# Kernel optimization log

Hardware: AMD Instinct MI355X
Metric: run time of the kernel (lower is better)

## Reference

```python
import jax, jax.numpy as jnp
import numpy as np

NSITES = 100000
NYEARS = 20
NVIS = 2
HDIM = 64


def setup_inputs() -> dict:
    key = jax.random.key(0)
    ks = jax.random.split(key, 10)
    def w(k, shape, fan_in):
        return (jax.random.normal(k, shape, jnp.float32) / np.sqrt(fan_in)).astype(jnp.float32)
    return {
        "sxy0": jax.random.normal(ks[0], (1, NSITES, 1), jnp.float32),
        "sxy": jax.random.normal(ks[1], (NSITES, NYEARS - 1, 1), jnp.float32),
        "oxy": jax.random.normal(ks[2], (NSITES, NYEARS, NVIS), jnp.float32),
        # to_h0: Linear(1 -> 64)
        "W_h0": w(ks[3], (HDIM, 1), 1), "b_h0": jnp.zeros((HDIM,), jnp.float32),
        # to_h1: Linear(64 -> 64)
        "W_h1": w(ks[4], (HDIM, HDIM), HDIM), "b_h1": jnp.zeros((HDIM,), jnp.float32),
        # to_hrnn: RNN(input=1, hidden=64, relu)
        "W_ih": w(ks[5], (HDIM, 1), 1), "b_ih": jnp.zeros((HDIM,), jnp.float32),
        "W_hh": w(ks[6], (HDIM, HDIM), HDIM), "b_hh": jnp.zeros((HDIM,), jnp.float32),
        # to_psi0 / to_psi: Linear(64 -> 1)
        "W_psi0": w(ks[7], (1, HDIM), HDIM), "b_psi0": jnp.zeros((1,), jnp.float32),
        "W_psi": w(ks[8], (1, HDIM), HDIM), "b_psi": jnp.zeros((1,), jnp.float32),
        # to_p: Linear(65 -> 1)
        "W_p": w(ks[9], (1, HDIM + 1), HDIM + 1), "b_p": jnp.zeros((1,), jnp.float32),
    }


def reference(sxy0, sxy, oxy, W_h0, b_h0, W_h1, b_h1, W_ih, b_ih, W_hh, b_hh,
              W_psi0, b_psi0, W_psi, b_psi, W_p, b_p):
    # site embeddings -> initial hidden state
    hs = jax.nn.elu(sxy0 @ W_h0.T + b_h0)            # [1, N, H]
    h0 = jax.nn.elu(hs @ W_h1.T + b_h1)              # [1, N, H]

    # single-layer relu RNN, batch_first: sxy [N, T, 1], h0 [1, N, H]
    xs = jnp.swapaxes(sxy, 0, 1)                     # [T, N, 1]
    def step(h, x):
        h_new = jax.nn.relu(x @ W_ih.T + b_ih + h @ W_hh.T + b_hh)
        return h_new, h_new
    _, h_seq = jax.lax.scan(step, h0[0], xs)         # [T, N, H]
    h_out = jnp.swapaxes(h_seq, 0, 1)                # [N, T, H]

    psi0_out = jax.nn.sigmoid(h0 @ W_psi0.T + b_psi0)   # [1, N, 1]
    psi_out = jax.nn.sigmoid(h_out @ W_psi.T + b_psi)   # [N, T, 1]

    # detection prob p[i, t, j] = sigmoid(to_p(cat(H[i, t], oxy[i, t, j])))
    # where H[:, 0] = h0 and H[:, t] = h_out[:, t-1] for t >= 1
    H = jnp.concatenate([h0[0][:, None, :], h_out], axis=1)  # [N, Y, H]
    logits = H @ W_p[:, :HDIM].T + oxy * W_p[0, HDIM] + b_p  # [N, Y, NVIS]
    p = jax.nn.sigmoid(logits)
    return psi0_out, psi_out, p
```

## Files before the change

kernel.cpp:

```cpp
#include <hip/hip_runtime.h>
#include <math.h>

#define NSITES 100000
#define NYEARS 20
#define HDIM 64
#define WSTR 72
#define SPB 128

typedef __bf16 bf16x8 __attribute__((ext_vector_type(8)));
typedef float f32x4 __attribute__((ext_vector_type(4)));

__device__ __forceinline__ float sigmoidf_(float x) { return 1.0f / (1.0f + __expf(-x)); }
__device__ __forceinline__ float eluf_(float x) { return x > 0.0f ? x : __expf(x) - 1.0f; }

__device__ __forceinline__ unsigned pack2_(float a, float b) {
    union { __bf16 h; unsigned short u; } x, y;
    x.h = (__bf16)a; y.h = (__bf16)b;
    return ((unsigned)y.u << 16) | (unsigned)x.u;
}

__device__ __forceinline__ bf16x8 cvt8_(const float* p) {
    float4 a = ((const float4*)p)[0];
    float4 b = ((const float4*)p)[1];
    bf16x8 r;
    r[0] = (__bf16)a.x; r[1] = (__bf16)a.y; r[2] = (__bf16)a.z; r[3] = (__bf16)a.w;
    r[4] = (__bf16)b.x; r[5] = (__bf16)b.y; r[6] = (__bf16)b.z; r[7] = (__bf16)b.w;
    return r;
}

__device__ __forceinline__ bf16x8 ldsfrag_(const unsigned short* b, int row, int off) {
    union { bf16x8 v; uint4 u; } r;
    r.u = *(const uint4*)&b[row * WSTR + off];
    return r.v;
}

__device__ __forceinline__ bf16x8 pack_bf_(f32x4 lo, f32x4 hi) {
    bf16x8 r;
    r[0] = (__bf16)lo[0]; r[1] = (__bf16)lo[1]; r[2] = (__bf16)lo[2]; r[3] = (__bf16)lo[3];
    r[4] = (__bf16)hi[0]; r[5] = (__bf16)hi[1]; r[6] = (__bf16)hi[2]; r[7] = (__bf16)hi[3];
    return r;
}

__global__ __launch_bounds__(512, 2)
void rnet_kernel(const float* __restrict__ sxy0,
                 const float* __restrict__ sxy,
                 const float* __restrict__ oxy,
                 const float* __restrict__ W_h0, const float* __restrict__ b_h0,
                 const float* __restrict__ W_h1, const float* __restrict__ b_h1,
                 const float* __restrict__ W_ih, const float* __restrict__ b_ih,
                 const float* __restrict__ W_hh, const float* __restrict__ b_hh,
                 const float* __restrict__ W_psi0, const float* __restrict__ b_psi0,
                 const float* __restrict__ W_psi, const float* __restrict__ b_psi,
                 const float* __restrict__ W_p, const float* __restrict__ b_p,
                 float* __restrict__ out)
{
    const int tid  = threadIdx.x;
    const int lane = tid & 63;
    const int wv   = tid >> 6;
    const int s = lane & 15;
    const int q = lane >> 4;
    const int sq = s >> 2, sr = s & 3;
    const int base = blockIdx.x * SPB;
    const int sl   = wv * 16 + s;
    const int site = base + sl;
    const int site_ld = site < NSITES ? site : NSITES - 1;

    __shared__ __align__(16) unsigned char region[SPB * 20 * 2 * 4];
    __shared__ __align__(16) float xs_sh[SPB * 19];
    unsigned short* const whh_l = (unsigned short*)region;
    unsigned short* const wh1_l = (unsigned short*)region + 64 * WSTR;
    float* const pL   = (float*)region;
    float* const psiL = (float*)region + SPB * 20;

    float* __restrict__ out_psi0 = out;
    float* __restrict__ out_psi  = out + NSITES;
    float* __restrict__ out_p    = out + 20 * NSITES;

    {
        const float4* whg = (const float4*)W_hh;
        const float4* w1g = (const float4*)W_h1;
#pragma unroll
        for (int j = 0; j < 2; ++j) {
            int e4 = j * 512 + tid;
            int row = e4 >> 4, c4 = e4 & 15;
            float4 a = whg[e4];
            uint2 pa; pa.x = pack2_(a.x, a.y); pa.y = pack2_(a.z, a.w);
            *(uint2*)&whh_l[row * WSTR + c4 * 4] = pa;
            float4 b = w1g[e4];
            uint2 pb; pb.x = pack2_(b.x, b.y); pb.y = pack2_(b.z, b.w);
            *(uint2*)&wh1_l[row * WSTR + c4 * 4] = pb;
        }
#pragma unroll
        for (int r = 0; r < 5; ++r) {
            int i = r * 512 + tid;
            if (i < SPB * 19) {
                int srow = i / 19, c = i - srow * 19;
                int gsite = base + srow; if (gsite >= NSITES) gsite = NSITES - 1;
                xs_sh[i] = sxy[(size_t)gsite * 19 + c];
            }
        }
    }
    __syncthreads();

    bf16x8 bf[2];
    {
        const float s0v = sxy0[site_ld];
        bf16x8 bf0[2];
#pragma unroll
        for (int kt = 0; kt < 2; ++kt) {
            const float* wp = W_h0 + kt * 32 + q * 8;
            const float* bp = b_h0 + kt * 32 + q * 8;
            float4 w0 = ((const float4*)wp)[0], w1 = ((const float4*)wp)[1];
            float4 c0 = ((const float4*)bp)[0], c1 = ((const float4*)bp)[1];
            float v[8];
            v[0] = eluf_(fmaf(s0v, w0.x, c0.x)); v[1] = eluf_(fmaf(s0v, w0.y, c0.y));
            v[2] = eluf_(fmaf(s0v, w0.z, c0.z)); v[3] = eluf_(fmaf(s0v, w0.w, c0.w));
            v[4] = eluf_(fmaf(s0v, w1.x, c1.x)); v[5] = eluf_(fmaf(s0v, w1.y, c1.y));
            v[6] = eluf_(fmaf(s0v, w1.z, c1.z)); v[7] = eluf_(fmaf(s0v, w1.w, c1.w));
#pragma unroll
            for (int j = 0; j < 8; ++j) bf0[kt][j] = (__bf16)v[j];
        }

        f32x4 acc[4];
#pragma unroll
        for (int mt = 0; mt < 4; ++mt) {
            const int dr = 32 * (mt >> 1) + 8 * q + 4 * (mt & 1);
            float4 b1 = *(const float4*)(b_h1 + dr);
            acc[mt][0] = b1.x; acc[mt][1] = b1.y; acc[mt][2] = b1.z; acc[mt][3] = b1.w;
        }
#pragma unroll
        for (int kt = 0; kt < 2; ++kt)
#pragma unroll
            for (int mt = 0; mt < 4; ++mt) {
                const int ar = 32 * (mt >> 1) + 8 * sq + 4 * (mt & 1) + sr;
                bf16x8 a = ldsfrag_(wh1_l, ar, kt * 32 + q * 8);
                acc[mt] = __builtin_amdgcn_mfma_f32_16x16x32_bf16(a, bf0[kt], acc[mt], 0, 0, 0);
            }
        f32x4 e[4];
#pragma unroll
        for (int mt = 0; mt < 4; ++mt)
#pragma unroll
            for (int r = 0; r < 4; ++r) e[mt][r] = eluf_(acc[mt][r]);
        bf[0] = pack_bf_(e[0], e[1]);
        bf[1] = pack_bf_(e[2], e[3]);
    }

    bf16x8 a_hh[4][2];
#pragma unroll
    for (int mt = 0; mt < 4; ++mt) {
        const int ar = 32 * (mt >> 1) + 8 * sq + 4 * (mt & 1) + sr;
#pragma unroll
        for (int kt = 0; kt < 2; ++kt)
            a_hh[mt][kt] = ldsfrag_(whh_l, ar, kt * 32 + q * 8);
    }

    __syncthreads();

    bf16x8 a_head[2];
    {
        const float* hrow = (s == 1) ? W_p : ((s == 2) ? W_psi0 : W_psi);
#pragma unroll
        for (int kt = 0; kt < 2; ++kt) a_head[kt] = cvt8_(hrow + kt * 32 + q * 8);
    }
    f32x4 biasD[4], wihD[4];
#pragma unroll
    for (int mt = 0; mt < 4; ++mt) {
        const int dr = 32 * (mt >> 1) + 8 * q + 4 * (mt & 1);
        float4 bi = *(const float4*)(b_ih + dr);
        float4 bh = *(const float4*)(b_hh + dr);
        float4 wi = *(const float4*)(W_ih + dr);
        biasD[mt][0] = bi.x + bh.x; biasD[mt][1] = bi.y + bh.y;
        biasD[mt][2] = bi.z + bh.z; biasD[mt][3] = bi.w + bh.w;
        wihD[mt][0] = wi.x; wihD[mt][1] = wi.y; wihD[mt][2] = wi.z; wihD[mt][3] = wi.w;
    }
    f32x4 headC;
    headC[0] = (q == 0) ? b_psi[0]  : 0.0f;
    headC[1] = (q == 0) ? b_p[0]    : 0.0f;
    headC[2] = (q == 0) ? b_psi0[0] : 0.0f;
    headC[3] = 0.0f;

    float x = xs_sh[sl * 19];
#pragma unroll 1
    for (int t = 1; t < NYEARS; ++t) {
        float x_next = (t < NYEARS - 1) ? xs_sh[sl * 19 + t] : 0.0f;

        f32x4 acc[4], accH;
#pragma unroll
        for (int mt = 0; mt < 4; ++mt)
            acc[mt] = __builtin_amdgcn_mfma_f32_16x16x32_bf16(a_hh[mt][0], bf[0], biasD[mt], 0, 0, 0);
        accH = __builtin_amdgcn_mfma_f32_16x16x32_bf16(a_head[0], bf[0], headC, 0, 0, 0);
#pragma unroll
        for (int mt = 0; mt < 4; ++mt)
            acc[mt] = __builtin_amdgcn_mfma_f32_16x16x32_bf16(a_hh[mt][1], bf[1], acc[mt], 0, 0, 0);
        accH = __builtin_amdgcn_mfma_f32_16x16x32_bf16(a_head[1], bf[1], accH, 0, 0, 0);

        f32x4 hn[4];
#pragma unroll
        for (int mt = 0; mt < 4; ++mt)
#pragma unroll
            for (int r = 0; r < 4; ++r)
                hn[mt][r] = fmaxf(fmaf(x, wihD[mt][r], acc[mt][r]), 0.0f);
        bf[0] = pack_bf_(hn[0], hn[1]);
        bf[1] = pack_bf_(hn[2], hn[3]);

        if (q == 0) {
            pL[sl * 20 + (t - 1)]   = accH[1];
            psiL[sl * 20 + (t - 1)] = accH[0];
            if (t == 1) psiL[sl * 20] = accH[2];
        }
        x = x_next;
    }

    {
        f32x4 accH = __builtin_amdgcn_mfma_f32_16x16x32_bf16(a_head[0], bf[0], headC, 0, 0, 0);
        accH = __builtin_amdgcn_mfma_f32_16x16x32_bf16(a_head[1], bf[1], accH, 0, 0, 0);
        if (q == 0) {
            pL[sl * 20 + 19]   = accH[1];
            psiL[sl * 20 + 19] = accH[0];
        }
    }

    __syncthreads();

    const float wpo = W_p[HDIM];
    if (tid < SPB && base + tid < NSITES) out_psi0[base + tid] = sigmoidf_(psiL[tid * 20]);
#pragma unroll
    for (int r = 0; r < 5; ++r) {
        int i = r * 512 + tid;
        if (i < SPB * 19 && (size_t)base * 19 + i < (size_t)NSITES * 19) {
            int s2 = i / 19, c = i - s2 * 19;
            out_psi[(size_t)base * 19 + i] = sigmoidf_(psiL[s2 * 20 + c + 1]);
        }
    }
    const float4* oxy_b = (const float4*)(oxy + (size_t)base * 40);
    float4* outp_b = (float4*)(out_p + (size_t)base * 40);
    const int p4max = (NSITES * 40) / 4;
#pragma unroll
    for (int r = 0; r < 3; ++r) {
        int i4 = r * 512 + tid;
        if (i4 < SPB * 10 && blockIdx.x * (SPB * 10) + i4 < p4max) {
            float4 ox = oxy_b[i4];
            float lg0 = pL[i4 * 2];
            float lg1 = pL[i4 * 2 + 1];
            float4 pv;
            pv.x = sigmoidf_(fmaf(wpo, ox.x, lg0));
            pv.y = sigmoidf_(fmaf(wpo, ox.y, lg0));
            pv.z = sigmoidf_(fmaf(wpo, ox.z, lg1));
            pv.w = sigmoidf_(fmaf(wpo, ox.w, lg1));
            outp_b[i4] = pv;
        }
    }
}

extern "C" void kernel_launch(void* const* d_in, const int* in_sizes, int n_in,
                              void* d_out, int out_size, void* d_ws, size_t ws_size,
                              hipStream_t stream) {
    const float* sxy0   = (const float*)d_in[0];
    const float* sxy    = (const float*)d_in[1];
    const float* oxy    = (const float*)d_in[2];
    const float* W_h0   = (const float*)d_in[3];
    const float* b_h0   = (const float*)d_in[4];
    const float* W_h1   = (const float*)d_in[5];
    const float* b_h1   = (const float*)d_in[6];
    const float* W_ih   = (const float*)d_in[7];
    const float* b_ih   = (const float*)d_in[8];
    const float* W_hh   = (const float*)d_in[9];
    const float* b_hh   = (const float*)d_in[10];
    const float* W_psi0 = (const float*)d_in[11];
    const float* b_psi0 = (const float*)d_in[12];
    const float* W_psi  = (const float*)d_in[13];
    const float* b_psi  = (const float*)d_in[14];
    const float* W_p    = (const float*)d_in[15];
    const float* b_p    = (const float*)d_in[16];

    float* out = (float*)d_out;

    dim3 block(512);
    dim3 grid((NSITES + SPB - 1) / SPB);
    rnet_kernel<<<grid, block, 0, stream>>>(
        sxy0, sxy, oxy, W_h0, b_h0, W_h1, b_h1, W_ih, b_ih, W_hh, b_hh,
        W_psi0, b_psi0, W_psi, b_psi, W_p, b_p, out);
}
```

Measured before the change: 146.7 us.

## Process two independent site groups per wave to interleave RNN recurrences

Halves the block to 256 threads so each wave handles two 16-site groups (A and B), running their recurrent MFMA chains interleaved within the same time step. The intent is to hide the dependent MFMA latency of the serial RNN recurrence by giving the scheduler independent work. Weight fragments in registers are shared between both groups, but register pressure roughly doubles for state and accumulators, and occupancy per block changes.

```diff
diff --git a/kernel.cpp b/kernel.cpp
--- a/kernel.cpp
+++ b/kernel.cpp
@@ -41,7 +41,7 @@
     return r;
 }
 
-__global__ __launch_bounds__(512, 2)
+__global__ __launch_bounds__(256, 4)
 void rnet_kernel(const float* __restrict__ sxy0,
                  const float* __restrict__ sxy,
                  const float* __restrict__ oxy,
@@ -61,9 +61,12 @@
     const int q = lane >> 4;
     const int sq = s >> 2, sr = s & 3;
     const int base = blockIdx.x * SPB;
-    const int sl   = wv * 16 + s;
-    const int site = base + sl;
-    const int site_ld = site < NSITES ? site : NSITES - 1;
+    const int slA  = wv * 16 + s;
+    const int slB  = slA + 64;
+    const int siteA = base + slA;
+    const int siteB = base + slB;
+    const int siteA_ld = siteA < NSITES ? siteA : NSITES - 1;
+    const int siteB_ld = siteB < NSITES ? siteB : NSITES - 1;
 
     __shared__ __align__(16) unsigned char region[SPB * 20 * 2 * 4];
     __shared__ __align__(16) float xs_sh[SPB * 19];
@@ -80,8 +83,8 @@
         const float4* whg = (const float4*)W_hh;
         const float4* w1g = (const float4*)W_h1;
 #pragma unroll
-        for (int j = 0; j < 2; ++j) {
-            int e4 = j * 512 + tid;
+        for (int j = 0; j < 4; ++j) {
+            int e4 = j * 256 + tid;
             int row = e4 >> 4, c4 = e4 & 15;
             float4 a = whg[e4];
             uint2 pa; pa.x = pack2_(a.x, a.y); pa.y = pack2_(a.z, a.w);
@@ -91,8 +94,8 @@
             *(uint2*)&wh1_l[row * WSTR + c4 * 4] = pb;
         }
 #pragma unroll
-        for (int r = 0; r < 5; ++r) {
-            int i = r * 512 + tid;
+        for (int r = 0; r < 10; ++r) {
+            int i = r * 256 + tid;
             if (i < SPB * 19) {
                 int srow = i / 19, c = i - srow * 19;
                 int gsite = base + srow; if (gsite >= NSITES) gsite = NSITES - 1;
@@ -102,31 +105,37 @@
     }
     __syncthreads();
 
-    bf16x8 bf[2];
-    {
-        const float s0v = sxy0[site_ld];
-        bf16x8 bf0[2];
+    bf16x8 bfA[2], bfB[2];
+    {
+        const float s0A = sxy0[siteA_ld];
+        const float s0B = sxy0[siteB_ld];
+        bf16x8 b0A[2], b0B[2];
 #pragma unroll
         for (int kt = 0; kt < 2; ++kt) {
             const float* wp = W_h0 + kt * 32 + q * 8;
             const float* bp = b_h0 + kt * 32 + q * 8;
             float4 w0 = ((const float4*)wp)[0], w1 = ((const float4*)wp)[1];
             float4 c0 = ((const float4*)bp)[0], c1 = ((const float4*)bp)[1];
-            float v[8];
-            v[0] = eluf_(fmaf(s0v, w0.x, c0.x)); v[1] = eluf_(fmaf(s0v, w0.y, c0.y));
-            v[2] = eluf_(fmaf(s0v, w0.z, c0.z)); v[3] = eluf_(fmaf(s0v, w0.w, c0.w));
-            v[4] = eluf_(fmaf(s0v, w1.x, c1.x)); v[5] = eluf_(fmaf(s0v, w1.y, c1.y));
-            v[6] = eluf_(fmaf(s0v, w1.z, c1.z)); v[7] = eluf_(fmaf(s0v, w1.w, c1.w));
-#pragma unroll
-            for (int j = 0; j < 8; ++j) bf0[kt][j] = (__bf16)v[j];
-        }
-
-        f32x4 acc[4];
+            float vA[8], vB[8];
+            vA[0] = eluf_(fmaf(s0A, w0.x, c0.x)); vA[1] = eluf_(fmaf(s0A, w0.y, c0.y));
+            vA[2] = eluf_(fmaf(s0A, w0.z, c0.z)); vA[3] = eluf_(fmaf(s0A, w0.w, c0.w));
+            vA[4] = eluf_(fmaf(s0A, w1.x, c1.x)); vA[5] = eluf_(fmaf(s0A, w1.y, c1.y));
+            vA[6] = eluf_(fmaf(s0A, w1.z, c1.z)); vA[7] = eluf_(fmaf(s0A, w1.w, c1.w));
+            vB[0] = eluf_(fmaf(s0B, w0.x, c0.x)); vB[1] = eluf_(fmaf(s0B, w0.y, c0.y));
+            vB[2] = eluf_(fmaf(s0B, w0.z, c0.z)); vB[3] = eluf_(fmaf(s0B, w0.w, c0.w));
+            vB[4] = eluf_(fmaf(s0B, w1.x, c1.x)); vB[5] = eluf_(fmaf(s0B, w1.y, c1.y));
+            vB[6] = eluf_(fmaf(s0B, w1.z, c1.z)); vB[7] = eluf_(fmaf(s0B, w1.w, c1.w));
+#pragma unroll
+            for (int j = 0; j < 8; ++j) { b0A[kt][j] = (__bf16)vA[j]; b0B[kt][j] = (__bf16)vB[j]; }
+        }
+
+        f32x4 accA[4], accB[4];
 #pragma unroll
         for (int mt = 0; mt < 4; ++mt) {
             const int dr = 32 * (mt >> 1) + 8 * q + 4 * (mt & 1);
             float4 b1 = *(const float4*)(b_h1 + dr);
-            acc[mt][0] = b1.x; acc[mt][1] = b1.y; acc[mt][2] = b1.z; acc[mt][3] = b1.w;
+            accA[mt][0] = b1.x; accA[mt][1] = b1.y; accA[mt][2] = b1.z; accA[mt][3] = b1.w;
+            accB[mt] = accA[mt];
         }
 #pragma unroll
         for (int kt = 0; kt < 2; ++kt)
@@ -134,15 +143,18 @@
             for (int mt = 0; mt < 4; ++mt) {
                 const int ar = 32 * (mt >> 1) + 8 * sq + 4 * (mt & 1) + sr;
                 bf16x8 a = ldsfrag_(wh1_l, ar, kt * 32 + q * 8);
-                acc[mt] = __builtin_amdgcn_mfma_f32_16x16x32_bf16(a, bf0[kt], acc[mt], 0, 0, 0);
+                accA[mt] = __builtin_amdgcn_mfma_f32_16x16x32_bf16(a, b0A[kt], accA[mt], 0, 0, 0);
+                accB[mt] = __builtin_amdgcn_mfma_f32_16x16x32_bf16(a, b0B[kt], accB[mt], 0, 0, 0);
             }
-        f32x4 e[4];
+        f32x4 eA[4], eB[4];
 #pragma unroll
         for (int mt = 0; mt < 4; ++mt)
 #pragma unroll
-            for (int r = 0; r < 4; ++r) e[mt][r] = eluf_(acc[mt][r]);
-        bf[0] = pack_bf_(e[0], e[1]);
-        bf[1] = pack_bf_(e[2], e[3]);
+            for (int r = 0; r < 4; ++r) { eA[mt][r] = eluf_(accA[mt][r]); eB[mt][r] = eluf_(accB[mt][r]); }
+        bfA[0] = pack_bf_(eA[0], eA[1]);
+        bfA[1] = pack_bf_(eA[2], eA[3]);
+        bfB[0] = pack_bf_(eB[0], eB[1]);
+        bfB[1] = pack_bf_(eB[2], eB[3]);
     }
 
     bf16x8 a_hh[4][2];
@@ -179,44 +191,78 @@
     headC[2] = (q == 0) ? b_psi0[0] : 0.0f;
     headC[3] = 0.0f;
 
-    float x = xs_sh[sl * 19];
+    float xA = xs_sh[slA * 19];
+    float xB = xs_sh[slB * 19];
 #pragma unroll 1
     for (int t = 1; t < NYEARS; ++t) {
-        float x_next = (t < NYEARS - 1) ? xs_sh[sl * 19 + t] : 0.0f;
-
-        f32x4 acc[4], accH;
-#pragma unroll
-        for (int mt = 0; mt < 4; ++mt)
-            acc[mt] = __builtin_amdgcn_mfma_f32_16x16x32_bf16(a_hh[mt][0], bf[0], biasD[mt], 0, 0, 0);
-        accH = __builtin_amdgcn_mfma_f32_16x16x32_bf16(a_head[0], bf[0], headC, 0, 0, 0);
-#pragma unroll
-        for (int mt = 0; mt < 4; ++mt)
-            acc[mt] = __builtin_amdgcn_mfma_f32_16x16x32_bf16(a_hh[mt][1], bf[1], acc[mt], 0, 0, 0);
-        accH = __builtin_amdgcn_mfma_f32_16x16x32_bf16(a_head[1], bf[1], accH, 0, 0, 0);
-
-        f32x4 hn[4];
-#pragma unroll
-        for (int mt = 0; mt < 4; ++mt)
-#pragma unroll
-            for (int r = 0; r < 4; ++r)
-                hn[mt][r] = fmaxf(fmaf(x, wihD[mt][r], acc[mt][r]), 0.0f);
-        bf[0] = pack_bf_(hn[0], hn[1]);
-        bf[1] = pack_bf_(hn[2], hn[3]);
-
+        float xAn = (t < NYEARS - 1) ? xs_sh[slA * 19 + t] : 0.0f;
+        float xBn = (t < NYEARS - 1) ? xs_sh[slB * 19 + t] : 0.0f;
+
+        {
+            f32x4 acc[4], accH;
+#pragma unroll
+            for (int mt = 0; mt < 4; ++mt)
+                acc[mt] = __builtin_amdgcn_mfma_f32_16x16x32_bf16(a_hh[mt][0], bfA[0], biasD[mt], 0, 0, 0);
+            accH = __builtin_amdgcn_mfma_f32_16x16x32_bf16(a_head[0], bfA[0], headC, 0, 0, 0);
+#pragma unroll
+            for (int mt = 0; mt < 4; ++mt)
+                acc[mt] = __builtin_amdgcn_mfma_f32_16x16x32_bf16(a_hh[mt][1], bfA[1], acc[mt], 0, 0, 0);
+            accH = __builtin_amdgcn_mfma_f32_16x16x32_bf16(a_head[1], bfA[1], accH, 0, 0, 0);
+            f32x4 hn[4];
+#pragma unroll
+            for (int mt = 0; mt < 4; ++mt)
+#pragma unroll
+                for (int r = 0; r < 4; ++r)
+                    hn[mt][r] = fmaxf(fmaf(xA, wihD[mt][r], acc[mt][r]), 0.0f);
+            bfA[0] = pack_bf_(hn[0], hn[1]);
+            bfA[1] = pack_bf_(hn[2], hn[3]);
+            if (q == 0) {
+                pL[slA * 20 + (t - 1)]   = accH[1];
+                psiL[slA * 20 + (t - 1)] = accH[0];
+                if (t == 1) psiL[slA * 20] = accH[2];
+            }
+        }
+        {
+            f32x4 acc[4], accH;
+#pragma unroll
+            for (int mt = 0; mt < 4; ++mt)
+                acc[mt] = __builtin_amdgcn_mfma_f32_16x16x32_bf16(a_hh[mt][0], bfB[0], biasD[mt], 0, 0, 0);
+            accH = __builtin_amdgcn_mfma_f32_16x16x32_bf16(a_head[0], bfB[0], headC, 0, 0, 0);
+#pragma unroll
+            for (int mt = 0; mt < 4; ++mt)
+                acc[mt] = __builtin_amdgcn_mfma_f32_16x16x32_bf16(a_hh[mt][1], bfB[1], acc[mt], 0, 0, 0);
+            accH = __builtin_amdgcn_mfma_f32_16x16x32_bf16(a_head[1], bfB[1], accH, 0, 0, 0);
+            f32x4 hn[4];
+#pragma unroll
+            for (int mt = 0; mt < 4; ++mt)
+#pragma unroll
+                for (int r = 0; r < 4; ++r)
+                    hn[mt][r] = fmaxf(fmaf(xB, wihD[mt][r], acc[mt][r]), 0.0f);
+            bfB[0] = pack_bf_(hn[0], hn[1]);
+            bfB[1] = pack_bf_(hn[2], hn[3]);
+            if (q == 0) {
+                pL[slB * 20 + (t - 1)]   = accH[1];
+                psiL[slB * 20 + (t - 1)] = accH[0];
+                if (t == 1) psiL[slB * 20] = accH[2];
+            }
+        }
+        xA = xAn; xB = xBn;
+    }
+
+    {
+        f32x4 accH = __builtin_amdgcn_mfma_f32_16x16x32_bf16(a_head[0], bfA[0], headC, 0, 0, 0);
+        accH = __builtin_amdgcn_mfma_f32_16x16x32_bf16(a_head[1], bfA[1], accH, 0, 0, 0);
         if (q == 0) {
-            pL[sl * 20 + (t - 1)]   = accH[1];
-            psiL[sl * 20 + (t - 1)] = accH[0];
-            if (t == 1) psiL[sl * 20] = accH[2];
-        }
-        x = x_next;
-    }
-
-    {
-        f32x4 accH = __builtin_amdgcn_mfma_f32_16x16x32_bf16(a_head[0], bf[0], headC, 0, 0, 0);
-        accH = __builtin_amdgcn_mfma_f32_16x16x32_bf16(a_head[1], bf[1], accH, 0, 0, 0);
+            pL[slA * 20 + 19]   = accH[1];
+            psiL[slA * 20 + 19] = accH[0];
+        }
+    }
+    {
+        f32x4 accH = __builtin_amdgcn_mfma_f32_16x16x32_bf16(a_head[0], bfB[0], headC, 0, 0, 0);
+        accH = __builtin_amdgcn_mfma_f32_16x16x32_bf16(a_head[1], bfB[1], accH, 0, 0, 0);
         if (q == 0) {
-            pL[sl * 20 + 19]   = accH[1];
-            psiL[sl * 20 + 19] = accH[0];
+            pL[slB * 20 + 19]   = accH[1];
+            psiL[slB * 20 + 19] = accH[0];
         }
     }
 
@@ -225,8 +271,8 @@
     const float wpo = W_p[HDIM];
     if (tid < SPB && base + tid < NSITES) out_psi0[base + tid] = sigmoidf_(psiL[tid * 20]);
 #pragma unroll
-    for (int r = 0; r < 5; ++r) {
-        int i = r * 512 + tid;
+    for (int r = 0; r < 10; ++r) {
+        int i = r * 256 + tid;
         if (i < SPB * 19 && (size_t)base * 19 + i < (size_t)NSITES * 19) {
             int s2 = i / 19, c = i - s2 * 19;
             out_psi[(size_t)base * 19 + i] = sigmoidf_(psiL[s2 * 20 + c + 1]);
@@ -236,8 +282,8 @@
     float4* outp_b = (float4*)(out_p + (size_t)base * 40);
     const int p4max = (NSITES * 40) / 4;
 #pragma unroll
-    for (int r = 0; r < 3; ++r) {
-        int i4 = r * 512 + tid;
+    for (int r = 0; r < 5; ++r) {
+        int i4 = r * 256 + tid;
         if (i4 < SPB * 10 && blockIdx.x * (SPB * 10) + i4 < p4max) {
             float4 ox = oxy_b[i4];
             float lg0 = pL[i4 * 2];
@@ -275,7 +321,7 @@
 
     float* out = (float*)d_out;
 
-    dim3 block(512);
+    dim3 block(256);
     dim3 grid((NSITES + SPB - 1) / SPB);
     rnet_kernel<<<grid, block, 0, stream>>>(
         sxy0, sxy, oxy, W_h0, b_h0, W_h1, b_h1, W_ih, b_ih, W_hh, b_hh,
```

After: 164.6 us. +12.2%, slower.
